# Performance work log

Measured on AMD Instinct MI355X. Metric: run time of the kernel, lower is better.

The kernel has to match this reference:

```python
import jax, jax.numpy as jnp
import numpy as np

N, D, T = 8192, 512, 12
EPS = 1e-6


def _ln(x, g, b):
    m = jnp.mean(x, axis=-1, keepdims=True)
    v = jnp.mean((x - m) ** 2, axis=-1, keepdims=True)
    return (x - m) / jnp.sqrt(v + EPS) * g + b


def _cross(x1, x2, Wa, ba, Wb, bb, d1, d2):
    # attn_weights2: [N, N], softmax over dim=1 (rows)
    aw2 = jax.nn.softmax((x1 @ Wa.T + ba) @ x2.T, axis=1)
    fused_x2 = (aw2 @ x2) / jnp.sqrt(jnp.float32(d2))
    aw1 = jax.nn.softmax((x2 @ Wb.T + bb) @ x1.T, axis=1)
    fused_x1 = (aw1 @ x1) / jnp.sqrt(jnp.float32(d1))
    return fused_x1, fused_x2


def setup_inputs() -> dict:
    key = jax.random.key(0)
    ks = jax.random.split(key, 16)
    s = 1.0 / np.sqrt(D)
    inp = {
        'xp': jax.random.normal(ks[0], (N, D), jnp.float32),
        'xm': jax.random.normal(ks[1], (N, D), jnp.float32),
        'xs': jax.random.normal(ks[2], (N, D), jnp.float32),
        'ln_g': jnp.ones((D,), jnp.float32),
        'ln_b': jnp.zeros((D,), jnp.float32),
        # mol cross-attention: linear1 (D->D), linear2 (D->D)
        'W1': jax.random.uniform(ks[3], (D, D), jnp.float32, -s, s),
        'b1': jnp.zeros((D,), jnp.float32),
        'W2': jax.random.uniform(ks[4], (D, D), jnp.float32, -s, s),
        'b2': jnp.zeros((D,), jnp.float32),
        # smile cross-attention
        'W3': jax.random.uniform(ks[5], (D, D), jnp.float32, -s, s),
        'b3': jnp.zeros((D,), jnp.float32),
        'W4': jax.random.uniform(ks[6], (D, D), jnp.float32, -s, s),
        'b4': jnp.zeros((D,), jnp.float32),
        # pred head: 2D -> T
        'Wp': jax.random.uniform(ks[7], (T, 2 * D), jnp.float32, -1.0 / np.sqrt(2 * D), 1.0 / np.sqrt(2 * D)),
        'bp': jnp.zeros((T,), jnp.float32),
        # gate
        't': jnp.full((1,), 0.5, jnp.float32),
        'Wt1': jax.random.uniform(ks[8], (50, 1), jnp.float32, -1.0, 1.0),
        'bt1': jnp.zeros((50,), jnp.float32),
        'Wt2': jax.random.uniform(ks[9], (1, 50), jnp.float32, -1.0 / np.sqrt(50), 1.0 / np.sqrt(50)),
        'bt2': jnp.zeros((1,), jnp.float32),
    }
    return inp


def reference(xp, xm, xs, ln_g, ln_b, W1, b1, W2, b2, W3, b3, W4, b4, Wp, bp, t, Wt1, bt1, Wt2, bt2):
    x1 = _ln(xp, ln_g, ln_b)
    x2 = _ln(xm, ln_g, ln_b)
    x3 = x1  # protein encoded twice with same LayerNorm
    x4 = _ln(xs, ln_g, ln_b)

    f1, f2 = _cross(x1, x2, W1, b1, W2, b2, D, D)
    h12 = jnp.concatenate([f1 + x1, f2 + x2], axis=1)          # [N, 2D]
    out12 = jax.nn.relu(h12) @ Wp.T + bp                        # [N, T]

    f3, f4 = _cross(x3, x4, W3, b3, W4, b4, D, D)
    h34 = jnp.concatenate([f3 + x3, f4 + x4], axis=1)
    out34 = jax.nn.relu(h34) @ Wp.T + bp

    t1 = t @ Wt1.T + bt1                                        # [50]
    t2 = jax.nn.sigmoid(t1 @ Wt2.T + bt2)                       # [1]
    return t2 * out12 + (1.0 - t2) * out34
```

## Files before the change

### kernel.cpp

```cpp
#include <hip/hip_runtime.h>
#include <stdint.h>


#define DEV __device__ __forceinline__
typedef unsigned short u16;
typedef __bf16 bf16x8 __attribute__((ext_vector_type(8)));
typedef float f32x4 __attribute__((ext_vector_type(4)));

constexpr int NR = 8192;
constexpr int DDIM = 512;
constexpr int TOUT = 12;

DEV u16 f2b(float f) {
  uint32_t u = __builtin_bit_cast(uint32_t, f);
  u += 0x7fffu + ((u >> 16) & 1u);
  return (u16)(u >> 16);
}
DEV float b2f(u16 h) {
  uint32_t u = ((uint32_t)h) << 16;
  return __builtin_bit_cast(float, u);
}

__global__ __launch_bounds__(64) void ln_kernel(
    const float* __restrict__ xp, const float* __restrict__ xm,
    const float* __restrict__ xs, const float* __restrict__ g,
    const float* __restrict__ b, u16* __restrict__ o1, u16* __restrict__ o2,
    u16* __restrict__ o4) {
  int row = blockIdx.x;
  int which = blockIdx.y;
  const float* x = which == 0 ? xp : (which == 1 ? xm : xs);
  u16* o = which == 0 ? o1 : (which == 1 ? o2 : o4);
  int lane = threadIdx.x;
  const float4* xr = (const float4*)(x + (size_t)row * DDIM);
  float4 v0 = xr[lane * 2], v1 = xr[lane * 2 + 1];
  float vals[8] = {v0.x, v0.y, v0.z, v0.w, v1.x, v1.y, v1.z, v1.w};
  float s = 0.f, s2 = 0.f;
  for (int j = 0; j < 8; j++) { s += vals[j]; s2 += vals[j] * vals[j]; }
  for (int off = 1; off < 64; off <<= 1) {
    s += __shfl_xor(s, off);
    s2 += __shfl_xor(s2, off);
  }
  float m = s * (1.0f / DDIM);
  float var = s2 * (1.0f / DDIM) - m * m;
  var = fmaxf(var, 0.f);
  float rs = rsqrtf(var + 1e-6f);
  int d0 = lane * 8;
  u16 us[8];
  for (int j = 0; j < 8; j++)
    us[j] = f2b((vals[j] - m) * rs * g[d0 + j] + b[d0 + j]);
  uint4 pk;
  pk.x = (uint32_t)us[0] | ((uint32_t)us[1] << 16);
  pk.y = (uint32_t)us[2] | ((uint32_t)us[3] << 16);
  pk.z = (uint32_t)us[4] | ((uint32_t)us[5] << 16);
  pk.w = (uint32_t)us[6] | ((uint32_t)us[7] << 16);
  *(uint4*)(o + (size_t)row * DDIM + d0) = pk;
}

__global__ __launch_bounds__(256) void wconv_kernel(
    const float* __restrict__ W1, const float* __restrict__ W2,
    const float* __restrict__ W3, const float* __restrict__ W4,
    u16* __restrict__ Wb) {
  int wi = blockIdx.y;
  const float* W = wi == 0 ? W1 : (wi == 1 ? W2 : (wi == 2 ? W3 : W4));
  size_t base = ((size_t)blockIdx.x * 256 + threadIdx.x) * 8;
  const float4* src = (const float4*)(W + base);
  float4 a = src[0], c = src[1];
  float vals[8] = {a.x, a.y, a.z, a.w, c.x, c.y, c.z, c.w};
  u16 us[8];
  for (int j = 0; j < 8; j++) us[j] = f2b(vals[j]);
  uint4 pk;
  pk.x = (uint32_t)us[0] | ((uint32_t)us[1] << 16);
  pk.y = (uint32_t)us[2] | ((uint32_t)us[3] << 16);
  pk.z = (uint32_t)us[4] | ((uint32_t)us[5] << 16);
  pk.w = (uint32_t)us[6] | ((uint32_t)us[7] << 16);
  *(uint4*)(Wb + (size_t)wi * DDIM * DDIM + base) = pk;
}

__global__ __launch_bounds__(256) void transpose_kernel(
    const u16* __restrict__ s1, const u16* __restrict__ s2,
    const u16* __restrict__ s4, u16* __restrict__ t1, u16* __restrict__ t2,
    u16* __restrict__ t4) {
  constexpr int LD = 66;
  __shared__ u16 tile[64 * LD];
  int which = blockIdx.z;
  const u16* src = which == 0 ? s1 : (which == 1 ? s2 : s4);
  u16* dst = which == 0 ? t1 : (which == 1 ? t2 : t4);
  int c0 = blockIdx.x * 64;
  int r0 = blockIdx.y * 64;
  int tid = threadIdx.x;
  for (int c = tid; c < 512; c += 256) {
    int i = c >> 3, j8 = (c & 7) * 8;
    uint4 v = *(const uint4*)(src + (size_t)(r0 + i) * DDIM + c0 + j8);
    uint32_t* dw = (uint32_t*)&tile[i * LD + j8];
    dw[0] = v.x; dw[1] = v.y; dw[2] = v.z; dw[3] = v.w;
  }
  __syncthreads();
  for (int rep = 0; rep < 2; rep++) {
    int idx = rep * 256 + tid;
    int o = idx >> 3, j8 = (idx & 7) * 8;
    u16 us[8];
    for (int k = 0; k < 8; k++) us[k] = tile[(j8 + k) * LD + o];
    uint4 pk;
    pk.x = (uint32_t)us[0] | ((uint32_t)us[1] << 16);
    pk.y = (uint32_t)us[2] | ((uint32_t)us[3] << 16);
    pk.z = (uint32_t)us[4] | ((uint32_t)us[5] << 16);
    pk.w = (uint32_t)us[6] | ((uint32_t)us[7] << 16);
    *(uint4*)(dst + (size_t)(c0 + o) * NR + r0 + j8) = pk;
  }
}

template <int MODE>
DEV void gemm_core(const u16* __restrict__ A, const u16* __restrict__ B,
                   u16* __restrict__ C, const float* __restrict__ bias,
                   u16* lds, int K, int lda, int ldb, int ldc, int bx,
                   int by) {
  constexpr int TM = 4, TN = 4;
  u16* Asm = lds;
  u16* Bsm = lds + 4096;
  int tid = threadIdx.x;
  int w = tid >> 6, lane = tid & 63;
  int q = lane >> 4, c16 = lane & 15;
  int n0 = bx * 128, m0 = by * 128;
  int wrow = (w >> 1) * 64, wcol = (w & 1) * 64;
  f32x4 acc[TM][TN] = {};
  for (int k0 = 0; k0 < K; k0 += 32) {
    __syncthreads();
    for (int call = w; call < 16; call += 4) {
      bool isA = call < 8;
      int ci = isA ? call : call - 8;
      int chunk = ci * 64 + lane;
      int row = chunk >> 2;
      int gch = ((chunk & 3) - (row >> 1)) & 3;
      const u16* gp = isA ? (A + (size_t)(m0 + row) * lda + k0 + gch * 8)
                          : (B + (size_t)(n0 + row) * ldb + k0 + gch * 8);
      u16* lp = (isA ? Asm : Bsm) + ci * 512;
      __builtin_amdgcn_global_load_lds(
          (const __attribute__((address_space(1))) void*)gp,
          (__attribute__((address_space(3))) void*)lp, 16, 0, 0);
    }
    __syncthreads();
    bf16x8 af[TM], bfr[TN];
    for (int i = 0; i < TM; i++) {
      int r = wrow + i * 16 + c16;
      af[i] = *(const bf16x8*)&Asm[r * 32 + (((q + (r >> 1)) & 3) * 8)];
    }
    for (int n = 0; n < TN; n++) {
      int r = wcol + n * 16 + c16;
      bfr[n] = *(const bf16x8*)&Bsm[r * 32 + (((q + (r >> 1)) & 3) * 8)];
    }
    for (int i = 0; i < TM; i++)
      for (int n = 0; n < TN; n++)
        acc[i][n] = __builtin_amdgcn_mfma_f32_16x16x32_bf16(af[i], bfr[n],
                                                            acc[i][n], 0, 0, 0);
  }
  for (int h = 0; h < 2; h++) {
    __syncthreads();
    if ((w & 1) == h) {
      for (int i = 0; i < TM; i++) {
        for (int n = 0; n < TN; n++) {
          float bv = 0.f;
          if constexpr (MODE == 0) bv = bias[n0 + wcol + n * 16 + c16];
          for (int r = 0; r < 4; r++) {
            int rl = wrow + i * 16 + q * 4 + r;
            int cl = (n * 16 + c16) ^ ((rl & 7) << 3);
            float v = acc[i][n][r];
            if constexpr (MODE == 0) v += bv;
            if constexpr (MODE == 1) v = __expf(v - 48.0f);
            lds[rl * 64 + cl] = f2b(v);
          }
        }
      }
    }
    __syncthreads();
    for (int rep = 0; rep < 4; rep++) {
      int idx = rep * 256 + tid;
      int row = idx >> 3, seg = idx & 7;
      uint4 vv = ((const uint4*)lds)[row * 8 + (seg ^ (row & 7))];
      *(uint4*)(C + (size_t)(m0 + row) * ldc + n0 + h * 64 + seg * 8) = vv;
    }
  }
}

DEV void pv_body(const u16* __restrict__ A, const u16* __restrict__ B,
                 u16* lds, u16* __restrict__ C, int bx, int by) {
  constexpr int BM = 64, BN = 128, BK = 64;
  int tid = threadIdx.x, w = tid >> 6, lane = tid & 63;
  int q = lane >> 4, c16 = lane & 15;
  int n0 = bx * BN, m0 = by * BM;
  int wr = (w >> 1) * 32, wc = (w & 1) * 64;
  f32x4 acc[2][4] = {};
  f32x4 accl[2] = {};
  bf16x8 ones;
  for (int j = 0; j < 8; j++) ones[j] = (__bf16)1.0f;

  auto stage = [&](int k0, int buf) {
    for (int it = 0; it < 6; it++) {
      int cb = it * 256 + w * 64;
      int c = cb + lane;
      bool isA = cb < 512;
      int ci = isA ? c : c - 512;
      int row = ci >> 3;
      int koff = ((ci & 7) ^ (row & 7)) * 8;
      const u16* gp = isA ? (A + (size_t)(m0 + row) * NR + k0 + koff)
                          : (B + (size_t)(n0 + row) * NR + k0 + koff);
      u16* lp = isA ? (lds + buf * 4096 + cb * 8)
                    : (lds + 8192 + buf * 8192 + (cb - 512) * 8);
      __builtin_amdgcn_global_load_lds(
          (const __attribute__((address_space(1))) void*)gp,
          (__attribute__((address_space(3))) void*)lp, 16, 0, 0);
    }
  };

  constexpr int KSTEPS = NR / BK;
  stage(0, 0);
  stage(BK, 1);
  for (int ks = 0; ks < KSTEPS; ks++) {
    int cur = ks & 1;
    if (ks + 1 < KSTEPS)
      asm volatile("s_waitcnt vmcnt(6)" ::: "memory");
    else
      asm volatile("s_waitcnt vmcnt(0)" ::: "memory");
    __builtin_amdgcn_sched_barrier(0);
    __builtin_amdgcn_s_barrier();
    __builtin_amdgcn_sched_barrier(0);
    const u16* Asm = lds + cur * 4096;
    const u16* Bsm = lds + 8192 + cur * 8192;
    for (int kh = 0; kh < 2; kh++) {
      bf16x8 af[2], bfr[4];
      int cl = kh * 4 + q;
      for (int i = 0; i < 2; i++) {
        int r = wr + i * 16 + c16;
        af[i] = *(const bf16x8*)&Asm[r * BK + ((cl ^ (r & 7)) * 8)];
      }
      for (int n = 0; n < 4; n++) {
        int r = wc + n * 16 + c16;
        bfr[n] = *(const bf16x8*)&Bsm[r * BK + ((cl ^ (r & 7)) * 8)];
      }
      for (int i = 0; i < 2; i++)
        accl[i] = __builtin_amdgcn_mfma_f32_16x16x32_bf16(af[i], ones, accl[i],
                                                          0, 0, 0);
      for (int i = 0; i < 2; i++)
        for (int n = 0; n < 4; n++)
          acc[i][n] = __builtin_amdgcn_mfma_f32_16x16x32_bf16(
              af[i], bfr[n], acc[i][n], 0, 0, 0);
    }
    asm volatile("s_waitcnt lgkmcnt(0)" ::: "memory");
    __builtin_amdgcn_sched_barrier(0);
    __builtin_amdgcn_s_barrier();
    __builtin_amdgcn_sched_barrier(0);
    if (ks + 2 < KSTEPS) stage((ks + 2) * BK, cur);
  }
  for (int i = 0; i < 2; i++) {
    float invl[4];
    for (int r = 0; r < 4; r++)
      invl[r] = 0.044194173824159216f / accl[i][r];
    for (int n = 0; n < 4; n++) {
      int col = n0 + wc + n * 16 + c16;
      for (int r = 0; r < 4; r++) {
        int row = m0 + wr + i * 16 + q * 4 + r;
        C[(size_t)row * DDIM + col] = f2b(acc[i][n][r] * invl[r]);
      }
    }
  }
}

__global__ __launch_bounds__(256, 4) void scores_kernel(
    const u16* __restrict__ Q, const u16* __restrict__ Kv,
    u16* __restrict__ P) {
  __shared__ u16 lds[8192];
  gemm_core<1>(Q, Kv, P, nullptr, lds, DDIM, DDIM, DDIM, NR, blockIdx.x,
               blockIdx.y);
}

__global__ __launch_bounds__(256, 4) void qproj_kernel(
    const u16* __restrict__ s0, const u16* __restrict__ s1,
    const u16* __restrict__ s2, const u16* __restrict__ s3,
    const u16* __restrict__ Wb, const float* __restrict__ b0,
    const float* __restrict__ b1, const float* __restrict__ b2,
    const float* __restrict__ b3, u16* __restrict__ Qs) {
  __shared__ u16 lds[8192];
  int z = blockIdx.z;
  const u16* A = z == 0 ? s0 : (z == 1 ? s1 : (z == 2 ? s2 : s3));
  const float* bias = z == 0 ? b0 : (z == 1 ? b1 : (z == 2 ? b2 : b3));
  gemm_core<0>(A, Wb + (size_t)z * DDIM * DDIM, Qs + (size_t)z * NR * DDIM,
               bias, lds, DDIM, DDIM, DDIM, DDIM, blockIdx.x, blockIdx.y);
}

__global__ __launch_bounds__(256, 4) void qscombo_kernel(
    const u16* __restrict__ x1b, const u16* __restrict__ x2b,
    const u16* __restrict__ x4b, const u16* __restrict__ Wb,
    const float* __restrict__ b1, const float* __restrict__ b2,
    const float* __restrict__ b3, u16* __restrict__ Qs,
    const u16* __restrict__ Q0, u16* __restrict__ P) {
  __shared__ u16 lds[8192];
  if (blockIdx.x < 768) {
    int b = blockIdx.x;
    int z = 1 + (b >> 8), rem = b & 255;
    const u16* A = z == 1 ? x2b : (z == 2 ? x1b : x4b);
    const float* bias = z == 1 ? b1 : (z == 2 ? b2 : b3);
    gemm_core<0>(A, Wb + (size_t)z * DDIM * DDIM, Qs + (size_t)z * NR * DDIM,
                 bias, lds, DDIM, DDIM, DDIM, DDIM, rem & 3, rem >> 2);
  } else {
    int b = blockIdx.x - 768;
    gemm_core<1>(Q0, x2b, P, nullptr, lds, DDIM, DDIM, DDIM, NR, b & 63,
                 b >> 6);
  }
}

__global__ __launch_bounds__(256, 3) void pv_kernel(
    const u16* __restrict__ A, const u16* __restrict__ B,
    u16* __restrict__ C) {
  __shared__ u16 lds[24576];
  pv_body(A, B, lds, C, blockIdx.x, blockIdx.y);
}

__global__ __launch_bounds__(256, 3) void combo_kernel(
    const u16* __restrict__ Pin, const u16* __restrict__ Vt,
    u16* __restrict__ F, const u16* __restrict__ Q,
    const u16* __restrict__ Kv, u16* __restrict__ Pout) {
  __shared__ u16 lds[24576];
  if (blockIdx.x < 512) {
    pv_body(Pin, Vt, lds, F, blockIdx.x & 3, blockIdx.x >> 2);
  } else {
    int b = blockIdx.x - 512;
    gemm_core<1>(Q, Kv, Pout, nullptr, lds, DDIM, DDIM, DDIM, NR, b & 63,
                 b >> 6);
  }
}

__global__ __launch_bounds__(256) void head_kernel(
    const u16* __restrict__ F1, const u16* __restrict__ F2,
    const u16* __restrict__ F3, const u16* __restrict__ F4,
    const u16* __restrict__ x1, const u16* __restrict__ x2,
    const u16* __restrict__ x4, const float* __restrict__ Wp,
    const float* __restrict__ bp, const float* __restrict__ tg,
    const float* __restrict__ Wt1, const float* __restrict__ bt1,
    const float* __restrict__ Wt2, const float* __restrict__ bt2,
    float* __restrict__ out) {
  __shared__ float wps[TOUT * 2 * DDIM];
  __shared__ float t2s;
  int tid = threadIdx.x;
  for (int i = tid; i < TOUT * 2 * DDIM; i += 256) wps[i] = Wp[i];
  if (tid == 0) {
    float s = bt2[0];
    for (int k = 0; k < 50; k++) s += Wt2[k] * (tg[0] * Wt1[k] + bt1[k]);
    t2s = 1.0f / (1.0f + __expf(-s));
  }
  __syncthreads();
  int g = tid >> 5, j = tid & 31;
  size_t m = (size_t)blockIdx.x * 8 + g;
  float a12[TOUT] = {}, a34[TOUT] = {};
  for (int d = j; d < 2 * DDIM; d += 32) {
    float h12, h34;
    if (d < DDIM) {
      float xv = b2f(x1[m * DDIM + d]);
      h12 = b2f(F1[m * DDIM + d]) + xv;
      h34 = b2f(F3[m * DDIM + d]) + xv;
    } else {
      int dd = d - DDIM;
      h12 = b2f(F2[m * DDIM + dd]) + b2f(x2[m * DDIM + dd]);
      h34 = b2f(F4[m * DDIM + dd]) + b2f(x4[m * DDIM + dd]);
    }
    h12 = fmaxf(h12, 0.f);
    h34 = fmaxf(h34, 0.f);
    for (int t = 0; t < TOUT; t++) {
      float wv = wps[t * 2 * DDIM + d];
      a12[t] += h12 * wv;
      a34[t] += h34 * wv;
    }
  }
  for (int off = 1; off < 32; off <<= 1)
    for (int t = 0; t < TOUT; t++) {
      a12[t] += __shfl_xor(a12[t], off);
      a34[t] += __shfl_xor(a34[t], off);
    }
  if (j < TOUT) {
    float t2 = t2s;
    out[m * TOUT + j] = t2 * a12[j] + (1.f - t2) * a34[j] + bp[j];
  }
}

extern "C" void kernel_launch(void* const* d_in, const int* in_sizes, int n_in,
                              void* d_out, int out_size, void* d_ws,
                              size_t ws_size, hipStream_t stream) {
  (void)in_sizes; (void)n_in; (void)out_size;
  const float* xp = (const float*)d_in[0];
  const float* xm = (const float*)d_in[1];
  const float* xs = (const float*)d_in[2];
  const float* ln_g = (const float*)d_in[3];
  const float* ln_b = (const float*)d_in[4];
  const float* Wmat[4] = {(const float*)d_in[5], (const float*)d_in[7],
                          (const float*)d_in[9], (const float*)d_in[11]};
  const float* bvec[4] = {(const float*)d_in[6], (const float*)d_in[8],
                          (const float*)d_in[10], (const float*)d_in[12]};
  const float* Wp = (const float*)d_in[13];
  const float* bp = (const float*)d_in[14];
  const float* tg = (const float*)d_in[15];
  const float* Wt1 = (const float*)d_in[16];
  const float* bt1 = (const float*)d_in[17];
  const float* Wt2 = (const float*)d_in[18];
  const float* bt2 = (const float*)d_in[19];
  float* out = (float*)d_out;

  char* ws = (char*)d_ws;
  const size_t MB = 1ull << 20;
  u16* x1b = (u16*)(ws + 0 * MB);
  u16* x2b = (u16*)(ws + 8 * MB);
  u16* x4b = (u16*)(ws + 16 * MB);
  u16* x1t = (u16*)(ws + 24 * MB);
  u16* x2t = (u16*)(ws + 32 * MB);
  u16* x4t = (u16*)(ws + 40 * MB);
  u16* Wb = (u16*)(ws + 48 * MB);
  u16* Qs = (u16*)(ws + 52 * MB);
  u16* P0 = (u16*)(ws + 84 * MB);
  bool dual = ws_size >= 340 * MB;
  u16* P1 = dual ? (u16*)(ws + 212 * MB) : P0;

  ln_kernel<<<dim3(NR, 3), 64, 0, stream>>>(xp, xm, xs, ln_g, ln_b, x1b, x2b,
                                            x4b);
  wconv_kernel<<<dim3(128, 4), 256, 0, stream>>>(Wmat[0], Wmat[1], Wmat[2],
                                                 Wmat[3], Wb);
  transpose_kernel<<<dim3(8, 128, 3), 256, 0, stream>>>(x1b, x2b, x4b, x1t,
                                                        x2t, x4t);
  qproj_kernel<<<dim3(DDIM / 128, NR / 128, 1), 256, 0, stream>>>(
      x1b, x2b, x1b, x4b, Wb, bvec[0], bvec[1], bvec[2], bvec[3], Qs);

  const u16* kvb[4] = {x2b, x1b, x4b, x1b};
  const u16* kvt[4] = {x2t, x1t, x4t, x1t};
  u16* slot[4];
  for (int a = 0; a < 4; a++) slot[a] = Qs + (size_t)a * NR * DDIM;

  qscombo_kernel<<<dim3(768 + 64 * 64), 256, 0, stream>>>(
      x1b, x2b, x4b, Wb, bvec[1], bvec[2], bvec[3], Qs, slot[0], P0);

  if (dual) {
    u16* Pb[4] = {P0, P1, P0, P1};
    for (int a = 0; a < 3; a++) {
      combo_kernel<<<dim3(512 + 64 * 64), 256, 0, stream>>>(
          Pb[a], kvt[a], slot[a], slot[a + 1], kvb[a + 1], Pb[a + 1]);
    }
    pv_kernel<<<dim3(4, 128), 256, 0, stream>>>(Pb[3], kvt[3], slot[3]);
  } else {
    for (int a = 0; a < 4; a++) {
      if (a > 0)
        scores_kernel<<<dim3(64, 64), 256, 0, stream>>>(slot[a], kvb[a], P0);
      pv_kernel<<<dim3(4, 128), 256, 0, stream>>>(P0, kvt[a], slot[a]);
    }
  }

  head_kernel<<<dim3(NR / 8), 256, 0, stream>>>(
      slot[1], slot[0], slot[3], slot[2], x1b, x2b, x4b, Wp, bp, tg, Wt1, bt1,
      Wt2, bt2, out);
}
```

Before: 995.7 us.

## Double-buffer gemm_core LDS staging and precompute load addresses in pv

gemm_core, used for the projections and attention scores, now double-buffers its A/B tiles in LDS with async global-to-LDS loads issued two steps ahead, using vmcnt waits and raw barriers in place of two __syncthreads per step. Shared memory for those kernels doubles to 32 KB. The per-lane global pointers and LDS offsets are computed once and advanced each step, and the same hoisting is applied to the pv kernel's staging. The aim is to overlap global load latency with MFMA work and cut address arithmetic, at the cost of more LDS per block, which may reduce occupancy.

```diff
diff --git a/kernel.cpp b/kernel.cpp
--- a/kernel.cpp
+++ b/kernel.cpp
@@ -115,43 +115,75 @@
                    u16* lds, int K, int lda, int ldb, int ldc, int bx,
                    int by) {
   constexpr int TM = 4, TN = 4;
-  u16* Asm = lds;
-  u16* Bsm = lds + 4096;
   int tid = threadIdx.x;
   int w = tid >> 6, lane = tid & 63;
   int q = lane >> 4, c16 = lane & 15;
   int n0 = bx * 128, m0 = by * 128;
   int wrow = (w >> 1) * 64, wcol = (w & 1) * 64;
+
+  const u16* gptr[4];
+  int lof[4];
+#pragma unroll
+  for (int j = 0; j < 4; j++) {
+    int call = w + j * 4;
+    bool isA = call < 8;
+    int ci = isA ? call : call - 8;
+    int chunk = ci * 64 + lane;
+    int row = chunk >> 2;
+    int gch = ((chunk & 3) - (row >> 1)) & 3;
+    gptr[j] = isA ? (A + (size_t)(m0 + row) * lda + gch * 8)
+                  : (B + (size_t)(n0 + row) * ldb + gch * 8);
+    lof[j] = (isA ? 0 : 4096) + ci * 512;
+  }
+  auto stageAll = [&](int buf) {
+    int bo = buf * 8192;
+#pragma unroll
+    for (int j = 0; j < 4; j++) {
+      __builtin_amdgcn_global_load_lds(
+          (const __attribute__((address_space(1))) void*)gptr[j],
+          (__attribute__((address_space(3))) void*)(lds + bo + lof[j]), 16, 0,
+          0);
+      gptr[j] += 32;
+    }
+  };
+
   f32x4 acc[TM][TN] = {};
-  for (int k0 = 0; k0 < K; k0 += 32) {
-    __syncthreads();
-    for (int call = w; call < 16; call += 4) {
-      bool isA = call < 8;
-      int ci = isA ? call : call - 8;
-      int chunk = ci * 64 + lane;
-      int row = chunk >> 2;
-      int gch = ((chunk & 3) - (row >> 1)) & 3;
-      const u16* gp = isA ? (A + (size_t)(m0 + row) * lda + k0 + gch * 8)
-                          : (B + (size_t)(n0 + row) * ldb + k0 + gch * 8);
-      u16* lp = (isA ? Asm : Bsm) + ci * 512;
-      __builtin_amdgcn_global_load_lds(
-          (const __attribute__((address_space(1))) void*)gp,
-          (__attribute__((address_space(3))) void*)lp, 16, 0, 0);
-    }
-    __syncthreads();
+  int nk = K >> 5;
+  stageAll(0);
+  stageAll(1);
+  for (int ks = 0; ks < nk; ks++) {
+    int cur = ks & 1;
+    if (ks + 1 < nk)
+      asm volatile("s_waitcnt vmcnt(4)" ::: "memory");
+    else
+      asm volatile("s_waitcnt vmcnt(0)" ::: "memory");
+    __builtin_amdgcn_sched_barrier(0);
+    __builtin_amdgcn_s_barrier();
+    __builtin_amdgcn_sched_barrier(0);
+    const u16* Asm = lds + cur * 8192;
+    const u16* Bsm = Asm + 4096;
     bf16x8 af[TM], bfr[TN];
+#pragma unroll
     for (int i = 0; i < TM; i++) {
       int r = wrow + i * 16 + c16;
       af[i] = *(const bf16x8*)&Asm[r * 32 + (((q + (r >> 1)) & 3) * 8)];
     }
+#pragma unroll
     for (int n = 0; n < TN; n++) {
       int r = wcol + n * 16 + c16;
       bfr[n] = *(const bf16x8*)&Bsm[r * 32 + (((q + (r >> 1)) & 3) * 8)];
     }
+#pragma unroll
     for (int i = 0; i < TM; i++)
+#pragma unroll
       for (int n = 0; n < TN; n++)
         acc[i][n] = __builtin_amdgcn_mfma_f32_16x16x32_bf16(af[i], bfr[n],
                                                             acc[i][n], 0, 0, 0);
+    asm volatile("s_waitcnt lgkmcnt(0)" ::: "memory");
+    __builtin_amdgcn_sched_barrier(0);
+    __builtin_amdgcn_s_barrier();
+    __builtin_amdgcn_sched_barrier(0);
+    if (ks + 2 < nk) stageAll(cur);
   }
   for (int h = 0; h < 2; h++) {
     __syncthreads();
@@ -193,27 +225,35 @@
   bf16x8 ones;
   for (int j = 0; j < 8; j++) ones[j] = (__bf16)1.0f;
 
-  auto stage = [&](int k0, int buf) {
+  const u16* gptr[6];
+  int lof0[6], lof1[6];
+#pragma unroll
+  for (int it = 0; it < 6; it++) {
+    int cb = it * 256 + w * 64;
+    int c = cb + lane;
+    bool isA = cb < 512;
+    int ci = isA ? c : c - 512;
+    int row = ci >> 3;
+    int koff = ((ci & 7) ^ (row & 7)) * 8;
+    gptr[it] = isA ? (A + (size_t)(m0 + row) * NR + koff)
+                   : (B + (size_t)(n0 + row) * NR + koff);
+    lof0[it] = isA ? (cb * 8) : (8192 + (cb - 512) * 8);
+    lof1[it] = isA ? (4096 + cb * 8) : (16384 + (cb - 512) * 8);
+  }
+  auto stage = [&](int buf) {
+#pragma unroll
     for (int it = 0; it < 6; it++) {
-      int cb = it * 256 + w * 64;
-      int c = cb + lane;
-      bool isA = cb < 512;
-      int ci = isA ? c : c - 512;
-      int row = ci >> 3;
-      int koff = ((ci & 7) ^ (row & 7)) * 8;
-      const u16* gp = isA ? (A + (size_t)(m0 + row) * NR + k0 + koff)
-                          : (B + (size_t)(n0 + row) * NR + k0 + koff);
-      u16* lp = isA ? (lds + buf * 4096 + cb * 8)
-                    : (lds + 8192 + buf * 8192 + (cb - 512) * 8);
+      int lo = buf ? lof1[it] : lof0[it];
       __builtin_amdgcn_global_load_lds(
-          (const __attribute__((address_space(1))) void*)gp,
-          (__attribute__((address_space(3))) void*)lp, 16, 0, 0);
+          (const __attribute__((address_space(1))) void*)gptr[it],
+          (__attribute__((address_space(3))) void*)(lds + lo), 16, 0, 0);
+      gptr[it] += BK;
     }
   };
 
   constexpr int KSTEPS = NR / BK;
-  stage(0, 0);
-  stage(BK, 1);
+  stage(0);
+  stage(1);
   for (int ks = 0; ks < KSTEPS; ks++) {
     int cur = ks & 1;
     if (ks + 1 < KSTEPS)
@@ -225,21 +265,27 @@
     __builtin_amdgcn_sched_barrier(0);
     const u16* Asm = lds + cur * 4096;
     const u16* Bsm = lds + 8192 + cur * 8192;
+#pragma unroll
     for (int kh = 0; kh < 2; kh++) {
       bf16x8 af[2], bfr[4];
       int cl = kh * 4 + q;
+#pragma unroll
       for (int i = 0; i < 2; i++) {
         int r = wr + i * 16 + c16;
         af[i] = *(const bf16x8*)&Asm[r * BK + ((cl ^ (r & 7)) * 8)];
       }
+#pragma unroll
       for (int n = 0; n < 4; n++) {
         int r = wc + n * 16 + c16;
         bfr[n] = *(const bf16x8*)&Bsm[r * BK + ((cl ^ (r & 7)) * 8)];
       }
+#pragma unroll
       for (int i = 0; i < 2; i++)
         accl[i] = __builtin_amdgcn_mfma_f32_16x16x32_bf16(af[i], ones, accl[i],
                                                           0, 0, 0);
+#pragma unroll
       for (int i = 0; i < 2; i++)
+#pragma unroll
         for (int n = 0; n < 4; n++)
           acc[i][n] = __builtin_amdgcn_mfma_f32_16x16x32_bf16(
               af[i], bfr[n], acc[i][n], 0, 0, 0);
@@ -248,7 +294,7 @@
     __builtin_amdgcn_sched_barrier(0);
     __builtin_amdgcn_s_barrier();
     __builtin_amdgcn_sched_barrier(0);
-    if (ks + 2 < KSTEPS) stage((ks + 2) * BK, cur);
+    if (ks + 2 < KSTEPS) stage(cur);
   }
   for (int i = 0; i < 2; i++) {
     float invl[4];
@@ -267,7 +313,7 @@
 __global__ __launch_bounds__(256, 4) void scores_kernel(
     const u16* __restrict__ Q, const u16* __restrict__ Kv,
     u16* __restrict__ P) {
-  __shared__ u16 lds[8192];
+  __shared__ u16 lds[16384];
   gemm_core<1>(Q, Kv, P, nullptr, lds, DDIM, DDIM, DDIM, NR, blockIdx.x,
                blockIdx.y);
 }
@@ -278,7 +324,7 @@
     const u16* __restrict__ Wb, const float* __restrict__ b0,
     const float* __restrict__ b1, const float* __restrict__ b2,
     const float* __restrict__ b3, u16* __restrict__ Qs) {
-  __shared__ u16 lds[8192];
+  __shared__ u16 lds[16384];
   int z = blockIdx.z;
   const u16* A = z == 0 ? s0 : (z == 1 ? s1 : (z == 2 ? s2 : s3));
   const float* bias = z == 0 ? b0 : (z == 1 ? b1 : (z == 2 ? b2 : b3));
@@ -292,7 +338,7 @@
     const float* __restrict__ b1, const float* __restrict__ b2,
     const float* __restrict__ b3, u16* __restrict__ Qs,
     const u16* __restrict__ Q0, u16* __restrict__ P) {
-  __shared__ u16 lds[8192];
+  __shared__ u16 lds[16384];
   if (blockIdx.x < 768) {
     int b = blockIdx.x;
     int z = 1 + (b >> 8), rem = b & 255;
```

After: 952.0 us. 4.4% less time.
